# Kernel tuning notes

Hardware: AMD Instinct MI355X
Metric: run time of the kernel (lower is better)

Reference implementation:

```python
import jax, jax.numpy as jnp
import numpy as np

NUM_USERS = 1_000_000
NUM_AGES = 8
NUM_ATTR = 40
FACE_K = 64
VISUAL_DIM = 2048
HIDDEN = 512
BATCH = 16384
VOCAB = NUM_USERS + 24 + 2 + NUM_AGES + NUM_ATTR  # fm_linear input width


def setup_inputs() -> dict:
    key = jax.random.key(0)
    ks = jax.random.split(key, 24)
    s = 0.02
    inp = {
        "user_id": jax.random.randint(ks[0], (BATCH,), 0, NUM_USERS),
        "hour": jax.random.randint(ks[1], (BATCH,), 0, 24),
        "visual": jax.random.normal(ks[2], (BATCH, VISUAL_DIM), jnp.float32),
        "scale": jax.random.uniform(ks[3], (BATCH, 1), jnp.float32),
        "gender": jax.random.randint(ks[4], (BATCH,), 0, 2),
        "age": jax.random.randint(ks[5], (BATCH,), 0, NUM_AGES),
        "attribute": jax.random.randint(ks[6], (BATCH,), 0, NUM_ATTR),
        # embedding tables
        "user_emb": jax.random.normal(ks[7], (NUM_USERS, FACE_K), jnp.float32) * s,
        "hour_emb": jax.random.normal(ks[8], (24, FACE_K), jnp.float32) * s,
        "gender_emb": jax.random.normal(ks[9], (2, FACE_K), jnp.float32) * s,
        "age_emb": jax.random.normal(ks[10], (NUM_AGES, FACE_K), jnp.float32) * s,
        "attr_emb": jax.random.normal(ks[11], (NUM_ATTR, FACE_K), jnp.float32) * s,
        # visual linear
        "visu_w": jax.random.normal(ks[12], (FACE_K, VISUAL_DIM), jnp.float32) * s,
        "visu_b": jnp.zeros((FACE_K,), jnp.float32),
        # fm linear over concatenated one-hots (width VOCAB, out 2)
        "fm_w": jax.random.normal(ks[13], (2, VOCAB), jnp.float32) * s,
        "fm_b": jnp.zeros((2,), jnp.float32),
        # dnn
        "w1": jax.random.normal(ks[14], (HIDDEN, 6 * FACE_K), jnp.float32) * s,
        "b1": jnp.zeros((HIDDEN,), jnp.float32),
        "w2": jax.random.normal(ks[15], (HIDDEN, HIDDEN), jnp.float32) * s,
        "b2": jnp.zeros((HIDDEN,), jnp.float32),
        "w3": jax.random.normal(ks[16], (2, HIDDEN), jnp.float32) * s,
        "b3": jnp.zeros((2,), jnp.float32),
    }
    return inp


def reference(user_id, hour, visual, scale, gender, age, attribute,
              user_emb, hour_emb, gender_emb, age_emb, attr_emb,
              visu_w, visu_b, fm_w, fm_b, w1, b1, w2, b2, w3, b3):
    B = user_id.shape[0]
    # fm linear: one_hot @ W^T == gather-sum of W columns at the hot indices
    cols = jnp.stack([
        user_id,
        NUM_USERS + hour,
        NUM_USERS + 24 + gender,
        NUM_USERS + 24 + 2 + age,
        NUM_USERS + 24 + 2 + NUM_AGES + attribute,
    ], axis=1)  # [B, 5]
    linear_part = fm_w[:, cols].sum(axis=2).T + fm_b  # [B, 2]

    # embeddings
    user = user_emb[user_id]            # [B, K]
    hr = hour_emb[hour]                 # [B, K]
    face = jnp.stack([gender_emb[gender], attr_emb[attribute], age_emb[age]], axis=1)  # [B,3,K]
    face = scale[:, None, :] * jnp.tanh(face)  # scale [B,1] -> [B,1,1]
    embeddings = jnp.concatenate([user[:, None, :], hr[:, None, :], face], axis=1)  # [B,5,K]

    # FM second order
    so = jnp.square(embeddings.sum(axis=1)) - jnp.square(embeddings).sum(axis=1)  # [B,K]
    second_order = 0.5 * so.sum(axis=1)  # [B]
    fm = linear_part + second_order[:, None]  # [B,2]

    # DNN
    vis = visual @ visu_w.T + visu_b  # [B,K]
    x = jnp.concatenate([embeddings.reshape(B, 5 * FACE_K), vis], axis=1)  # [B,6K]
    x = jax.nn.relu(x @ w1.T + b1)
    x = jax.nn.relu(x @ w2.T + b2)
    x = x @ w3.T + b3
    return jax.nn.softmax(fm + x, axis=1)
```

## Files before the change

kernel.cpp:

```cpp
#include <hip/hip_runtime.h>
#include <hip/hip_bf16.h>
#include <stdint.h>

#define BATCH 16384
#define FACE_K 64
#define VISUAL_DIM 2048
#define HIDDEN 512
#define NUM_USERS 1000000
#define NUM_AGES 8
#define NUM_ATTR 40
#define VOCAB (NUM_USERS + 24 + 2 + NUM_AGES + NUM_ATTR)
#define XDIM 384

typedef __bf16 bf16x8 __attribute__((ext_vector_type(8)));
typedef float f32x4 __attribute__((ext_vector_type(4)));

__device__ __forceinline__ uint16_t f2bf(float f) {
    union { float f; uint32_t u; } v; v.f = f;
    uint32_t r = v.u + 0x7fffu + ((v.u >> 16) & 1u);
    return (uint16_t)(r >> 16);
}
__device__ __forceinline__ float bf2f(uint16_t h) {
    union { uint32_t u; float f; } v; v.u = ((uint32_t)h) << 16;
    return v.f;
}

__global__ void cvt_f32_bf16(const float* __restrict__ src, uint16_t* __restrict__ dst, int n4) {
    int i = blockIdx.x * blockDim.x + threadIdx.x;
    if (i < n4) {
        float4 v = ((const float4*)src)[i];
        ushort4 o;
        o.x = f2bf(v.x); o.y = f2bf(v.y); o.z = f2bf(v.z); o.w = f2bf(v.w);
        ((ushort4*)dst)[i] = o;
    }
}

__global__ void embed_fm_kernel(const int* __restrict__ uid, const int* __restrict__ hour,
                                const float* __restrict__ scale, const int* __restrict__ gender,
                                const int* __restrict__ age, const int* __restrict__ attr,
                                const float* __restrict__ user_emb, const float* __restrict__ hour_emb,
                                const float* __restrict__ gender_emb, const float* __restrict__ age_emb,
                                const float* __restrict__ attr_emb,
                                const float* __restrict__ fm_w, const float* __restrict__ fm_b,
                                uint16_t* __restrict__ x, float* __restrict__ fm) {
    int row = blockIdx.x * 4 + (threadIdx.x >> 6);
    int lane = threadIdx.x & 63;
    int u = uid[row], h = hour[row], g = gender[row], a = age[row], at = attr[row];
    float sc = scale[row];
    float eu  = user_emb[(size_t)u * 64 + lane];
    float eh  = hour_emb[h * 64 + lane];
    float eg  = sc * tanhf(gender_emb[g * 64 + lane]);
    float eat = sc * tanhf(attr_emb[at * 64 + lane]);
    float eag = sc * tanhf(age_emb[a * 64 + lane]);
    float s  = eu + eh + eg + eat + eag;
    float sq = eu*eu + eh*eh + eg*eg + eat*eat + eag*eag;
    float so = s * s - sq;
    float l0 = 0.f, l1 = 0.f;
    if (lane < 5) {
        int col = (lane == 0) ? u
                : (lane == 1) ? (NUM_USERS + h)
                : (lane == 2) ? (NUM_USERS + 24 + g)
                : (lane == 3) ? (NUM_USERS + 26 + a)
                :               (NUM_USERS + 34 + at);
        l0 = fm_w[col];
        l1 = fm_w[VOCAB + col];
    }
    for (int m = 32; m; m >>= 1) {
        so += __shfl_xor(so, m);
        l0 += __shfl_xor(l0, m);
        l1 += __shfl_xor(l1, m);
    }
    if (lane == 0) {
        fm[row * 2 + 0] = l0 + fm_b[0] + 0.5f * so;
        fm[row * 2 + 1] = l1 + fm_b[1] + 0.5f * so;
    }
    size_t xb = (size_t)row * XDIM;
    x[xb +       lane] = f2bf(eu);
    x[xb +  64 + lane] = f2bf(eh);
    x[xb + 128 + lane] = f2bf(eg);
    x[xb + 192 + lane] = f2bf(eat);
    x[xb + 256 + lane] = f2bf(eag);
}

__global__ __launch_bounds__(256) void visual_gemm(const float* __restrict__ visual,
                                                   const uint16_t* __restrict__ Wb,
                                                   const float* __restrict__ bias,
                                                   uint16_t* __restrict__ x) {
    __shared__ uint16_t sA[64][72];
    __shared__ uint16_t sB[64][72];
    int t = threadIdx.x;
    int m0 = blockIdx.x * 64;
    int wv = t >> 6, lane = t & 63;
    int quad = lane >> 4, lc = lane & 15;

    f32x4 acc[4];
    #pragma unroll
    for (int j = 0; j < 4; ++j) acc[j] = (f32x4){0.f, 0.f, 0.f, 0.f};

    for (int k0 = 0; k0 < VISUAL_DIM; k0 += 64) {
        __syncthreads();
        #pragma unroll
        for (int p = 0; p < 4; ++p) {
            int idx = t + p * 256;
            int r = idx >> 4, q = idx & 15;
            float4 v = *(const float4*)(visual + (size_t)(m0 + r) * VISUAL_DIM + k0 + q * 4);
            ushort4 o; o.x = f2bf(v.x); o.y = f2bf(v.y); o.z = f2bf(v.z); o.w = f2bf(v.w);
            *(ushort4*)(&sA[r][q * 4]) = o;
        }
        #pragma unroll
        for (int p = 0; p < 2; ++p) {
            int idx = t + p * 256;
            int r = idx >> 3, q = idx & 7;
            uint4 v = *(const uint4*)(Wb + (size_t)r * VISUAL_DIM + k0 + q * 8);
            *(uint4*)(&sB[r][q * 8]) = v;
        }
        __syncthreads();
        const uint16_t* pa = &sA[wv * 16 + lc][0];
        #pragma unroll
        for (int ks = 0; ks < 2; ++ks) {
            bf16x8 af = *(const bf16x8*)(pa + ks * 32 + quad * 8);
            #pragma unroll
            for (int j = 0; j < 4; ++j) {
                bf16x8 bf = *(const bf16x8*)(&sB[j * 16 + lc][ks * 32 + quad * 8]);
                acc[j] = __builtin_amdgcn_mfma_f32_16x16x32_bf16(af, bf, acc[j], 0, 0, 0);
            }
        }
    }
    #pragma unroll
    for (int j = 0; j < 4; ++j) {
        int col = j * 16 + lc;
        float b = bias[col];
        #pragma unroll
        for (int r = 0; r < 4; ++r) {
            int row = m0 + wv * 16 + quad * 4 + r;
            x[(size_t)row * XDIM + 320 + col] = f2bf(acc[j][r] + b);
        }
    }
}

template <int KTOT, bool RELU>
__global__ __launch_bounds__(256) void gemm_bf16(const uint16_t* __restrict__ A,
                                                 const uint16_t* __restrict__ W,
                                                 const float* __restrict__ bias,
                                                 uint16_t* __restrict__ C, int ldc) {
    __shared__ uint16_t sA[64][72];
    __shared__ uint16_t sB[64][72];
    int t = threadIdx.x;
    int m0 = blockIdx.x * 64;
    int n0 = blockIdx.y * 64;
    int wv = t >> 6, lane = t & 63;
    int quad = lane >> 4, lc = lane & 15;

    f32x4 acc[4];
    #pragma unroll
    for (int j = 0; j < 4; ++j) acc[j] = (f32x4){0.f, 0.f, 0.f, 0.f};

    for (int k0 = 0; k0 < KTOT; k0 += 64) {
        __syncthreads();
        #pragma unroll
        for (int p = 0; p < 2; ++p) {
            int idx = t + p * 256;
            int r = idx >> 3, q = idx & 7;
            uint4 va = *(const uint4*)(A + (size_t)(m0 + r) * KTOT + k0 + q * 8);
            *(uint4*)(&sA[r][q * 8]) = va;
            uint4 vb = *(const uint4*)(W + (size_t)(n0 + r) * KTOT + k0 + q * 8);
            *(uint4*)(&sB[r][q * 8]) = vb;
        }
        __syncthreads();
        const uint16_t* pa = &sA[wv * 16 + lc][0];
        #pragma unroll
        for (int ks = 0; ks < 2; ++ks) {
            bf16x8 af = *(const bf16x8*)(pa + ks * 32 + quad * 8);
            #pragma unroll
            for (int j = 0; j < 4; ++j) {
                bf16x8 bf = *(const bf16x8*)(&sB[j * 16 + lc][ks * 32 + quad * 8]);
                acc[j] = __builtin_amdgcn_mfma_f32_16x16x32_bf16(af, bf, acc[j], 0, 0, 0);
            }
        }
    }
    #pragma unroll
    for (int j = 0; j < 4; ++j) {
        int col = n0 + j * 16 + lc;
        float b = bias[col];
        #pragma unroll
        for (int r = 0; r < 4; ++r) {
            int row = m0 + wv * 16 + quad * 4 + r;
            float v = acc[j][r] + b;
            if (RELU) v = fmaxf(v, 0.f);
            C[(size_t)row * ldc + col] = f2bf(v);
        }
    }
}

__global__ void final_kernel(const uint16_t* __restrict__ h2, const float* __restrict__ w3,
                             const float* __restrict__ b3, const float* __restrict__ fm,
                             float* __restrict__ out) {
    int row = blockIdx.x * 4 + (threadIdx.x >> 6);
    int lane = threadIdx.x & 63;
    uint4 hv = *(const uint4*)(h2 + (size_t)row * HIDDEN + lane * 8);
    const uint16_t* hp = (const uint16_t*)&hv;
    float4 wa0 = *(const float4*)(w3 + lane * 8);
    float4 wb0 = *(const float4*)(w3 + lane * 8 + 4);
    float4 wa1 = *(const float4*)(w3 + HIDDEN + lane * 8);
    float4 wb1 = *(const float4*)(w3 + HIDDEN + lane * 8 + 4);
    float hf[8];
    #pragma unroll
    for (int j = 0; j < 8; ++j) hf[j] = bf2f(hp[j]);
    float d0 = hf[0]*wa0.x + hf[1]*wa0.y + hf[2]*wa0.z + hf[3]*wa0.w
             + hf[4]*wb0.x + hf[5]*wb0.y + hf[6]*wb0.z + hf[7]*wb0.w;
    float d1 = hf[0]*wa1.x + hf[1]*wa1.y + hf[2]*wa1.z + hf[3]*wa1.w
             + hf[4]*wb1.x + hf[5]*wb1.y + hf[6]*wb1.z + hf[7]*wb1.w;
    for (int m = 32; m; m >>= 1) {
        d0 += __shfl_xor(d0, m);
        d1 += __shfl_xor(d1, m);
    }
    if (lane == 0) {
        float l0 = fm[row * 2 + 0] + d0 + b3[0];
        float l1 = fm[row * 2 + 1] + d1 + b3[1];
        float mx = fmaxf(l0, l1);
        float e0 = __expf(l0 - mx), e1 = __expf(l1 - mx);
        float inv = 1.f / (e0 + e1);
        out[row * 2 + 0] = e0 * inv;
        out[row * 2 + 1] = e1 * inv;
    }
}

extern "C" void kernel_launch(void* const* d_in, const int* in_sizes, int n_in,
                              void* d_out, int out_size, void* d_ws, size_t ws_size,
                              hipStream_t stream) {
    const int*   user_id   = (const int*)d_in[0];
    const int*   hour      = (const int*)d_in[1];
    const float* visual    = (const float*)d_in[2];
    const float* scale     = (const float*)d_in[3];
    const int*   gender    = (const int*)d_in[4];
    const int*   age       = (const int*)d_in[5];
    const int*   attribute = (const int*)d_in[6];
    const float* user_emb  = (const float*)d_in[7];
    const float* hour_emb  = (const float*)d_in[8];
    const float* gender_emb= (const float*)d_in[9];
    const float* age_emb   = (const float*)d_in[10];
    const float* attr_emb  = (const float*)d_in[11];
    const float* visu_w    = (const float*)d_in[12];
    const float* visu_b    = (const float*)d_in[13];
    const float* fm_w      = (const float*)d_in[14];
    const float* fm_b      = (const float*)d_in[15];
    const float* w1        = (const float*)d_in[16];
    const float* b1        = (const float*)d_in[17];
    const float* w2        = (const float*)d_in[18];
    const float* b2        = (const float*)d_in[19];
    const float* w3        = (const float*)d_in[20];
    const float* b3        = (const float*)d_in[21];
    float* out = (float*)d_out;

    char* ws = (char*)d_ws;
    uint16_t* x   = (uint16_t*)ws;
    uint16_t* h1  = (uint16_t*)(ws + 12582912);
    uint16_t* h2  = (uint16_t*)(ws + 12582912 + 16777216);
    float*    fm  = (float*)   (ws + 12582912 + 2 * 16777216);
    uint16_t* vwb = (uint16_t*)(ws + 12582912 + 2 * 16777216 + 131072);
    uint16_t* w1b = vwb + 64 * 2048;
    uint16_t* w2b = w1b + 512 * 384;

    {
        int n4 = 64 * 2048 / 4;
        cvt_f32_bf16<<<(n4 + 255) / 256, 256, 0, stream>>>(visu_w, vwb, n4);
        n4 = 512 * 384 / 4;
        cvt_f32_bf16<<<(n4 + 255) / 256, 256, 0, stream>>>(w1, w1b, n4);
        n4 = 512 * 512 / 4;
        cvt_f32_bf16<<<(n4 + 255) / 256, 256, 0, stream>>>(w2, w2b, n4);
    }
    embed_fm_kernel<<<BATCH / 4, 256, 0, stream>>>(user_id, hour, scale, gender, age, attribute,
                                                   user_emb, hour_emb, gender_emb, age_emb,
                                                   attr_emb, fm_w, fm_b, x, fm);
    visual_gemm<<<BATCH / 64, 256, 0, stream>>>(visual, vwb, visu_b, x);
    gemm_bf16<XDIM, true><<<dim3(BATCH / 64, 8), 256, 0, stream>>>(x, w1b, b1, h1, HIDDEN);
    gemm_bf16<HIDDEN, true><<<dim3(BATCH / 64, 8), 256, 0, stream>>>(h1, w2b, b2, h2, HIDDEN);
    final_kernel<<<BATCH / 4, 256, 0, stream>>>(h2, w3, b3, fm, out);
}
```

Before: 525.1 us.

## Replace LDS-tiled GEMMs with direct-register MFMA loads and split-K visual GEMM

The visual GEMM now uses 16-row blocks of two waves. Each wave handles half of K, loading fp32 activations straight from global memory into MFMA registers, and the two partial sums are combined through shared memory. The two DNN GEMMs drop shared-memory staging and the __syncthreads barriers; each wave loads its A and B fragments directly from global memory. This removes LDS traffic and barrier stalls and gives the visual GEMM more blocks, at the cost of losing intra-block reuse of the weight tiles and relying on L1/L2 caching for the repeated loads.

```diff
diff --git a/kernel.cpp b/kernel.cpp
--- a/kernel.cpp
+++ b/kernel.cpp
@@ -82,100 +82,80 @@
     x[xb + 256 + lane] = f2bf(eag);
 }
 
-__global__ __launch_bounds__(256) void visual_gemm(const float* __restrict__ visual,
+__global__ __launch_bounds__(128) void visual_gemm(const float* __restrict__ visual,
                                                    const uint16_t* __restrict__ Wb,
                                                    const float* __restrict__ bias,
                                                    uint16_t* __restrict__ x) {
-    __shared__ uint16_t sA[64][72];
-    __shared__ uint16_t sB[64][72];
-    int t = threadIdx.x;
-    int m0 = blockIdx.x * 64;
-    int wv = t >> 6, lane = t & 63;
-    int quad = lane >> 4, lc = lane & 15;
+    __shared__ float red[64 * 16];
+    int wv = threadIdx.x >> 6, lane = threadIdx.x & 63;
+    int lc = lane & 15, quad = lane >> 4;
+    int m0 = blockIdx.x * 16;
+
+    const float*    ap = visual + (size_t)(m0 + lc) * VISUAL_DIM + quad * 8 + wv * 1024;
+    const uint16_t* wp = Wb + (size_t)lc * VISUAL_DIM + quad * 8 + wv * 1024;
 
     f32x4 acc[4];
     #pragma unroll
     for (int j = 0; j < 4; ++j) acc[j] = (f32x4){0.f, 0.f, 0.f, 0.f};
 
-    for (int k0 = 0; k0 < VISUAL_DIM; k0 += 64) {
-        __syncthreads();
-        #pragma unroll
-        for (int p = 0; p < 4; ++p) {
-            int idx = t + p * 256;
-            int r = idx >> 4, q = idx & 15;
-            float4 v = *(const float4*)(visual + (size_t)(m0 + r) * VISUAL_DIM + k0 + q * 4);
-            ushort4 o; o.x = f2bf(v.x); o.y = f2bf(v.y); o.z = f2bf(v.z); o.w = f2bf(v.w);
-            *(ushort4*)(&sA[r][q * 4]) = o;
-        }
-        #pragma unroll
-        for (int p = 0; p < 2; ++p) {
-            int idx = t + p * 256;
-            int r = idx >> 3, q = idx & 7;
-            uint4 v = *(const uint4*)(Wb + (size_t)r * VISUAL_DIM + k0 + q * 8);
-            *(uint4*)(&sB[r][q * 8]) = v;
-        }
-        __syncthreads();
-        const uint16_t* pa = &sA[wv * 16 + lc][0];
-        #pragma unroll
-        for (int ks = 0; ks < 2; ++ks) {
-            bf16x8 af = *(const bf16x8*)(pa + ks * 32 + quad * 8);
+    #pragma unroll 2
+    for (int k = 0; k < 1024; k += 32) {
+        float4 a0 = *(const float4*)(ap + k);
+        float4 a1 = *(const float4*)(ap + k + 4);
+        bf16x8 af;
+        af[0] = (__bf16)a0.x; af[1] = (__bf16)a0.y; af[2] = (__bf16)a0.z; af[3] = (__bf16)a0.w;
+        af[4] = (__bf16)a1.x; af[5] = (__bf16)a1.y; af[6] = (__bf16)a1.z; af[7] = (__bf16)a1.w;
+        #pragma unroll
+        for (int j = 0; j < 4; ++j) {
+            bf16x8 bf = *(const bf16x8*)(wp + (size_t)(j * 16) * VISUAL_DIM + k);
+            acc[j] = __builtin_amdgcn_mfma_f32_16x16x32_bf16(af, bf, acc[j], 0, 0, 0);
+        }
+    }
+    if (wv == 1) {
+        #pragma unroll
+        for (int j = 0; j < 4; ++j)
+            *(f32x4*)(&red[lane * 16 + j * 4]) = acc[j];
+    }
+    __syncthreads();
+    if (wv == 0) {
+        #pragma unroll
+        for (int j = 0; j < 4; ++j) {
+            f32x4 o = *(const f32x4*)(&red[lane * 16 + j * 4]);
+            int col = j * 16 + lc;
+            float b = bias[col];
             #pragma unroll
-            for (int j = 0; j < 4; ++j) {
-                bf16x8 bf = *(const bf16x8*)(&sB[j * 16 + lc][ks * 32 + quad * 8]);
-                acc[j] = __builtin_amdgcn_mfma_f32_16x16x32_bf16(af, bf, acc[j], 0, 0, 0);
+            for (int r = 0; r < 4; ++r) {
+                int row = m0 + quad * 4 + r;
+                x[(size_t)row * XDIM + 320 + col] = f2bf(acc[j][r] + o[r] + b);
             }
         }
     }
-    #pragma unroll
-    for (int j = 0; j < 4; ++j) {
-        int col = j * 16 + lc;
-        float b = bias[col];
-        #pragma unroll
-        for (int r = 0; r < 4; ++r) {
-            int row = m0 + wv * 16 + quad * 4 + r;
-            x[(size_t)row * XDIM + 320 + col] = f2bf(acc[j][r] + b);
-        }
-    }
 }
 
 template <int KTOT, bool RELU>
-__global__ __launch_bounds__(256) void gemm_bf16(const uint16_t* __restrict__ A,
-                                                 const uint16_t* __restrict__ W,
-                                                 const float* __restrict__ bias,
-                                                 uint16_t* __restrict__ C, int ldc) {
-    __shared__ uint16_t sA[64][72];
-    __shared__ uint16_t sB[64][72];
-    int t = threadIdx.x;
-    int m0 = blockIdx.x * 64;
+__global__ __launch_bounds__(256) void gemm_direct(const uint16_t* __restrict__ A,
+                                                   const uint16_t* __restrict__ W,
+                                                   const float* __restrict__ bias,
+                                                   uint16_t* __restrict__ C, int ldc) {
+    int wv = threadIdx.x >> 6, lane = threadIdx.x & 63;
+    int lc = lane & 15, quad = lane >> 4;
+    int m0 = blockIdx.x * 64 + wv * 16;
     int n0 = blockIdx.y * 64;
-    int wv = t >> 6, lane = t & 63;
-    int quad = lane >> 4, lc = lane & 15;
+
+    const uint16_t* ap = A + (size_t)(m0 + lc) * KTOT + quad * 8;
+    const uint16_t* wp = W + (size_t)(n0 + lc) * KTOT + quad * 8;
 
     f32x4 acc[4];
     #pragma unroll
     for (int j = 0; j < 4; ++j) acc[j] = (f32x4){0.f, 0.f, 0.f, 0.f};
 
-    for (int k0 = 0; k0 < KTOT; k0 += 64) {
-        __syncthreads();
-        #pragma unroll
-        for (int p = 0; p < 2; ++p) {
-            int idx = t + p * 256;
-            int r = idx >> 3, q = idx & 7;
-            uint4 va = *(const uint4*)(A + (size_t)(m0 + r) * KTOT + k0 + q * 8);
-            *(uint4*)(&sA[r][q * 8]) = va;
-            uint4 vb = *(const uint4*)(W + (size_t)(n0 + r) * KTOT + k0 + q * 8);
-            *(uint4*)(&sB[r][q * 8]) = vb;
-        }
-        __syncthreads();
-        const uint16_t* pa = &sA[wv * 16 + lc][0];
-        #pragma unroll
-        for (int ks = 0; ks < 2; ++ks) {
-            bf16x8 af = *(const bf16x8*)(pa + ks * 32 + quad * 8);
-            #pragma unroll
-            for (int j = 0; j < 4; ++j) {
-                bf16x8 bf = *(const bf16x8*)(&sB[j * 16 + lc][ks * 32 + quad * 8]);
-                acc[j] = __builtin_amdgcn_mfma_f32_16x16x32_bf16(af, bf, acc[j], 0, 0, 0);
-            }
+    #pragma unroll 2
+    for (int k = 0; k < KTOT; k += 32) {
+        bf16x8 af = *(const bf16x8*)(ap + k);
+        #pragma unroll
+        for (int j = 0; j < 4; ++j) {
+            bf16x8 bf = *(const bf16x8*)(wp + (size_t)(j * 16) * KTOT + k);
+            acc[j] = __builtin_amdgcn_mfma_f32_16x16x32_bf16(af, bf, acc[j], 0, 0, 0);
         }
     }
     #pragma unroll
@@ -184,7 +164,7 @@
         float b = bias[col];
         #pragma unroll
         for (int r = 0; r < 4; ++r) {
-            int row = m0 + wv * 16 + quad * 4 + r;
+            int row = m0 + quad * 4 + r;
             float v = acc[j][r] + b;
             if (RELU) v = fmaxf(v, 0.f);
             C[(size_t)row * ldc + col] = f2bf(v);
@@ -272,8 +252,8 @@
     embed_fm_kernel<<<BATCH / 4, 256, 0, stream>>>(user_id, hour, scale, gender, age, attribute,
                                                    user_emb, hour_emb, gender_emb, age_emb,
                                                    attr_emb, fm_w, fm_b, x, fm);
-    visual_gemm<<<BATCH / 64, 256, 0, stream>>>(visual, vwb, visu_b, x);
-    gemm_bf16<XDIM, true><<<dim3(BATCH / 64, 8), 256, 0, stream>>>(x, w1b, b1, h1, HIDDEN);
-    gemm_bf16<HIDDEN, true><<<dim3(BATCH / 64, 8), 256, 0, stream>>>(h1, w2b, b2, h2, HIDDEN);
+    visual_gemm<<<BATCH / 16, 128, 0, stream>>>(visual, vwb, visu_b, x);
+    gemm_direct<XDIM, true><<<dim3(BATCH / 64, 8), 256, 0, stream>>>(x, w1b, b1, h1, HIDDEN);
+    gemm_direct<HIDDEN, true><<<dim3(BATCH / 64, 8), 256, 0, stream>>>(h1, w2b, b2, h2, HIDDEN);
     final_kernel<<<BATCH / 4, 256, 0, stream>>>(h2, w3, b3, fm, out);
 }
```

Measured after the change: 572.7 us. +9.1%, slower.
